# Performance work log

Measured on AMD Instinct MI355X. Metric: run time of the kernel, lower is better.

## Reference

```python
import jax, jax.numpy as jnp
import numpy as np
import math

B, S, D, H = 2, 2048, 1024, 16
HD = D // H            # head dim = 64
E, K = 8, 2            # routed experts, top-k
HM = 1024              # moe_inter_dim (multiple_of=256 keeps it)
HS = 1024              # shared expert hidden = moe_inter_dim * n_shared_experts
EPS = 1e-6
TEMP = 1.0


def setup_inputs() -> dict:
    key = jax.random.key(0)
    ks = jax.random.split(key, 16)
    s = 0.02
    x = jax.random.normal(ks[0], (B, S, D), jnp.float32)
    # RoPE angles: theta = 10000
    inv_freq = 1.0 / (10000.0 ** (np.arange(0, HD, 2, dtype=np.float32) / HD))  # (HD//2,)
    ang = np.arange(S, dtype=np.float32)[:, None] * inv_freq[None, :]           # (S, HD//2)
    freqs_cos = jnp.asarray(np.cos(ang))
    freqs_sin = jnp.asarray(np.sin(ang))
    return {
        "x": x,
        "freqs_cos": freqs_cos,
        "freqs_sin": freqs_sin,
        "att_norm_w": jnp.ones((D,), jnp.float32),
        "ffn_norm_w": jnp.ones((D,), jnp.float32),
        "wq": jax.random.normal(ks[1], (D, D), jnp.float32) * s,
        "wk": jax.random.normal(ks[2], (D, D), jnp.float32) * s,
        "wv": jax.random.normal(ks[3], (D, D), jnp.float32) * s,
        "wo": jax.random.normal(ks[4], (D, D), jnp.float32) * s,
        "gate_w": jax.random.normal(ks[5], (E, D), jnp.float32) * s,
        "ew1": jax.random.normal(ks[6], (E, D, HM), jnp.float32) * s,
        "ew2": jax.random.normal(ks[7], (E, HM, D), jnp.float32) * s,
        "ew3": jax.random.normal(ks[8], (E, D, HM), jnp.float32) * s,
        "sw1": jax.random.normal(ks[9], (D, HS), jnp.float32) * s,
        "sw2": jax.random.normal(ks[10], (HS, D), jnp.float32) * s,
        "sw3": jax.random.normal(ks[11], (D, HS), jnp.float32) * s,
    }


def _rmsnorm(x, w):
    return x * jax.lax.rsqrt(jnp.mean(x * x, axis=-1, keepdims=True) + EPS) * w


def _rope(t, cos, sin):
    # t: (B,H,S,HD); rotate pairs (even, odd) like complex multiply
    tr = t.reshape(B, H, S, HD // 2, 2)
    t0, t1 = tr[..., 0], tr[..., 1]
    c = cos[None, None, :, :]
    s_ = sin[None, None, :, :]
    o0 = t0 * c - t1 * s_
    o1 = t0 * s_ + t1 * c
    return jnp.stack([o0, o1], axis=-1).reshape(B, H, S, HD)


def reference(x, freqs_cos, freqs_sin, att_norm_w, ffn_norm_w,
              wq, wk, wv, wo, gate_w, ew1, ew2, ew3, sw1, sw2, sw3):
    # ---- attention sub-block ----
    xn = _rmsnorm(x, att_norm_w)
    q = (xn @ wq).reshape(B, S, H, HD).transpose(0, 2, 1, 3)  # (B,H,S,HD)
    k = (xn @ wk).reshape(B, S, H, HD).transpose(0, 2, 1, 3)
    v = (xn @ wv).reshape(B, S, H, HD).transpose(0, 2, 1, 3)
    q = _rope(q, freqs_cos, freqs_sin)
    k = _rope(k, freqs_cos, freqs_sin)
    scores = jnp.einsum('bhqd,bhkd->bhqk', q, k) / math.sqrt(HD)
    attn = jax.nn.softmax(scores, axis=-1)
    out = jnp.einsum('bhqk,bhkd->bhqd', attn, v)
    out = out.transpose(0, 2, 1, 3).reshape(B, S, D) @ wo
    h = x + out

    # ---- MoE sub-block ----
    xf = _rmsnorm(h, ffn_norm_w).reshape(-1, D)  # (N,D), N=B*S
    # shared expert (SwiGLU)
    shared = (jax.nn.silu(xf @ sw1) * (xf @ sw3)) @ sw2
    # gate (eval mode: no noise)
    g_scores = (xf @ gate_w.T) / TEMP
    probs = jax.nn.softmax(g_scores, axis=-1)          # (N,E)
    vals, idx = jax.lax.top_k(probs, K)                 # (N,K)
    vals = vals / (jnp.sum(vals, axis=-1, keepdims=True) + 1e-9)
    # per-token per-expert weight (equivalent to scatter into expert_mask)
    mask = jnp.sum(jax.nn.one_hot(idx, E, dtype=xf.dtype) * vals[..., None], axis=1)  # (N,E)
    # routed experts: dense per-expert SwiGLU, weighted combine (zero weight => no contribution)
    h1 = jax.nn.silu(jnp.einsum('nd,edh->enh', xf, ew1)) * jnp.einsum('nd,edh->enh', xf, ew3)
    eo = jnp.einsum('enh,ehd->end', h1, ew2)            # (E,N,D)
    y = jnp.einsum('end,ne->nd', eo, mask) + shared
    return h + y.reshape(B, S, D)
```

## Files before the change

kernel.cpp:

```cpp
#include <hip/hip_runtime.h>
#include <hip/hip_bf16.h>
#include <stdint.h>


typedef __hip_bfloat16 bf16;
typedef __attribute__((ext_vector_type(8))) __bf16 bf16x8;
typedef __attribute__((ext_vector_type(4))) float f32x4;
typedef __attribute__((ext_vector_type(2))) unsigned int u32x2;

#define S_  2048
#define D_  1024
#define N_  4096
#define HM_ 1024
#define HS_ 1024

__device__ __forceinline__ float b2f(bf16 h) { return __bfloat162float(h); }
__device__ __forceinline__ bf16  f2b(float f) { return __float2bfloat16(f); }

__device__ __forceinline__ bf16x8 ld_bf16x8(const bf16* p) {
    union { uint4 u; bf16x8 v; } x;
    x.u = *(const uint4*)p;
    return x.v;
}

__device__ __forceinline__ void gload_lds16(const void* gsrc, void* ldst) {
    __builtin_amdgcn_global_load_lds(
        (__attribute__((address_space(1))) void*)const_cast<void*>(gsrc),
        (__attribute__((address_space(3))) void*)ldst, 16, 0, 0);
}

__device__ __forceinline__ u32x2 tr16_read(unsigned lds_off) {
    u32x2 d;
    asm volatile("ds_read_b64_tr_b16 %0, %1" : "=v"(d) : "v"(lds_off));
    return d;
}

__global__ __launch_bounds__(256)
void transpose_cvt(const float* __restrict__ in, bf16* __restrict__ out,
                   int ld_in, int ld_out, int rowmul, int rowoff,
                   long in_bstride, long out_bstride)
{
    __shared__ float t[32][33];
    const int e = blockIdx.z;
    in  += (size_t)e * in_bstride;
    out += (size_t)e * out_bstride;
    const int c0 = blockIdx.x * 32, r0 = blockIdx.y * 32;
    const int tx = threadIdx.x & 31, ty = threadIdx.x >> 5;
#pragma unroll
    for (int i = 0; i < 32; i += 8)
        t[ty + i][tx] = in[(size_t)(r0 + ty + i) * ld_in + c0 + tx];
    __syncthreads();
#pragma unroll
    for (int i = 0; i < 32; i += 8)
        out[(size_t)((c0 + ty + i) * rowmul + rowoff) * ld_out + r0 + tx] = f2b(t[tx][ty + i]);
}

__global__ __launch_bounds__(256)
void rmsnorm_kernel(const float* __restrict__ x, const float* __restrict__ w,
                    bf16* __restrict__ out)
{
    const int n = blockIdx.x;
    const int tid = threadIdx.x;
    const float4 v = *(const float4*)(x + (size_t)n * D_ + tid * 4);
    float ss = v.x * v.x + v.y * v.y + v.z * v.z + v.w * v.w;
#pragma unroll
    for (int m = 1; m < 64; m <<= 1) ss += __shfl_xor(ss, m);
    __shared__ float red[4];
    if ((tid & 63) == 0) red[tid >> 6] = ss;
    __syncthreads();
    const float tot = red[0] + red[1] + red[2] + red[3];
    const float rstd = rsqrtf(tot * (1.0f / D_) + 1e-6f);
    const float4 wv = *(const float4*)(w + tid * 4);
    union { bf16 h[4]; uint2 u; } pk;
    pk.h[0] = f2b(v.x * rstd * wv.x);
    pk.h[1] = f2b(v.y * rstd * wv.y);
    pk.h[2] = f2b(v.z * rstd * wv.z);
    pk.h[3] = f2b(v.w * rstd * wv.w);
    *(uint2*)(out + (size_t)n * D_ + tid * 4) = pk.u;
}

template<int EPI, int MODE>
__global__ __launch_bounds__(256)
void gemm_bt(const bf16* __restrict__ A, const bf16* __restrict__ Bt,
             void* __restrict__ Cout, const float* __restrict__ resid,
             int M, int Kdim, int lda, int ldb, int ldc, long bstride,
             const int* __restrict__ tlist, const int* __restrict__ offs)
{
    __shared__ bf16 As[128 * 32];
    __shared__ bf16 Bs[128 * 32];
    const int tid = threadIdx.x;
    const int wave = tid >> 6, lane = tid & 63;

    int mcount = M, outBase = 0;
    const bf16* Bp = Bt;
    if (MODE != 0) {
        const int e = blockIdx.z;
        outBase = offs[e];
        mcount = offs[e + 1] - outBase;
        Bp = Bt + (size_t)e * bstride;
    }
    const int m0 = blockIdx.y * 128;
    if (m0 >= mcount) return;
    const int n0 = blockIdx.x * 128;

    const int srow = tid >> 2;
    const int scol = (tid & 3) * 8;
    const bf16* aptr[2];
    const bf16* bptr[2];
#pragma unroll
    for (int i = 0; i < 2; i++) {
        int r = m0 + i * 64 + srow;
        if (r >= mcount) r = mcount - 1;
        long arow;
        if (MODE == 1)      arow = tlist[outBase + r];
        else if (MODE == 2) arow = (long)outBase + r;
        else                arow = r;
        aptr[i] = A + (size_t)arow * lda + scol;
        bptr[i] = Bp + (size_t)(n0 + i * 64 + srow) * ldb + scol;
    }

    f32x4 zero4 = {0.f, 0.f, 0.f, 0.f};
    f32x4 acc[4][4];
#pragma unroll
    for (int m = 0; m < 4; m++)
#pragma unroll
        for (int n = 0; n < 4; n++) acc[m][n] = zero4;

    const int wm = (wave >> 1) * 64, wn = (wave & 1) * 64;
    const int fr = lane & 15, fk = (lane >> 4) * 8;
    const int aoff = (wm + fr) * 32 + fk;
    const int boff = (wn + fr) * 32 + fk;

    for (int kt = 0; kt < Kdim; kt += 32) {
        __syncthreads();
#pragma unroll
        for (int i = 0; i < 2; i++) {
            gload_lds16(aptr[i] + kt, (char*)As + i * 4096 + wave * 1024);
            gload_lds16(bptr[i] + kt, (char*)Bs + i * 4096 + wave * 1024);
        }
        __syncthreads();
        bf16x8 af[4], bfr[4];
#pragma unroll
        for (int m = 0; m < 4; m++) af[m] = ld_bf16x8(&As[aoff + m * 512]);
#pragma unroll
        for (int n = 0; n < 4; n++) bfr[n] = ld_bf16x8(&Bs[boff + n * 512]);
#pragma unroll
        for (int m = 0; m < 4; m++)
#pragma unroll
            for (int n = 0; n < 4; n++)
                acc[m][n] = __builtin_amdgcn_mfma_f32_16x16x32_bf16(af[m], bfr[n], acc[m][n], 0, 0, 0);
    }

    const int crow = m0 + wm + (lane >> 4) * 4;
    const int ccol = n0 + wn + fr;
#pragma unroll
    for (int m = 0; m < 4; m++)
#pragma unroll
        for (int n = 0; n < 4; n++)
#pragma unroll
            for (int j = 0; j < 4; j++) {
                const int r = crow + m * 16 + j;
                const int c = ccol + n * 16;
                const float v = acc[m][n][j];
                if (EPI == 3) {
                    const float other = __shfl_xor(v, 1);
                    const float res = (v / (1.f + __expf(-v))) * other;
                    if (((lane & 1) == 0) && r < mcount)
                        ((bf16*)Cout)[(size_t)(outBase + r) * ldc + (c >> 1)] = f2b(res);
                } else if (r < mcount) {
                    const size_t oi = (size_t)(outBase + r) * ldc + c;
                    if (EPI == 0)      ((bf16*)Cout)[oi] = f2b(v);
                    else if (EPI == 1) ((float*)Cout)[oi] = v;
                    else               ((float*)Cout)[oi] = resid[oi] + v;
                }
            }
}

__global__ __launch_bounds__(256)
void rope_kernel(bf16* __restrict__ qkv, const float* __restrict__ fc, const float* __restrict__ fs)
{
    const int n = blockIdx.x;
    const int s = n & (S_ - 1);
    bf16* row = qkv + (size_t)n * 3072;
    for (int p = threadIdx.x; p < 1024; p += 256) {
        const int sec = p >> 9;
        const int idx = p & 511;
        const int hh = idx >> 5, j = idx & 31;
        const int col = sec * 1024 + hh * 64 + 2 * j;
        const float c = fc[s * 32 + j], si = fs[s * 32 + j];
        const float v0 = b2f(row[col]), v1 = b2f(row[col + 1]);
        float o0 = v0 * c - v1 * si;
        float o1 = v0 * si + v1 * c;
        if (sec == 0) { o0 *= 0.125f; o1 *= 0.125f; }
        row[col] = f2b(o0);
        row[col + 1] = f2b(o1);
    }
}

__global__ __launch_bounds__(256)
void attn_kernel(const bf16* __restrict__ qkv, bf16* __restrict__ out)
{
    __shared__ __align__(16) bf16 Ks[64 * 72];
    __shared__ __align__(16) bf16 Vs[4 * 1032 + 8];
    const int tid = threadIdx.x, wave = tid >> 6, lane = tid & 63;
    const int b = blockIdx.z, hh = blockIdx.y;
    const int q0 = blockIdx.x * 128;
    const bf16* base  = qkv + ((size_t)b * S_) * 3072 + (size_t)hh * 64;
    const bf16* kbase = base + 1024;
    const bf16* vbase = base + 2048;
    const int fr = lane & 15, fg = lane >> 4;

    bf16x8 aq[2][2];
#pragma unroll
    for (int qb = 0; qb < 2; qb++)
#pragma unroll
        for (int s2 = 0; s2 < 2; s2++)
            aq[qb][s2] = ld_bf16x8(base + (size_t)(q0 + wave * 32 + qb * 16 + fr) * 3072 + s2 * 32 + fg * 8);

    f32x4 zero4 = {0.f, 0.f, 0.f, 0.f};
    f32x4 acc_o[2][4];
    float mrow[2], lrow[2];
#pragma unroll
    for (int qb = 0; qb < 2; qb++) {
#pragma unroll
        for (int hf = 0; hf < 4; hf++) acc_o[qb][hf] = zero4;
        mrow[qb] = -1e30f; lrow[qb] = 0.f;
    }

    const int srow = tid >> 2, sc4 = tid & 3;
    const unsigned vtr0 =
        (unsigned)(uintptr_t)(__attribute__((address_space(3))) void*)&Vs[0] + lane * 8;

    uint4 kg0, kg1, vg0, vg1;
    {
        const bf16* kr = kbase + (size_t)srow * 3072 + sc4 * 16;
        kg0 = *(const uint4*)kr; kg1 = *(const uint4*)(kr + 8);
        const bf16* vr = vbase + (size_t)srow * 3072 + sc4 * 16;
        vg0 = *(const uint4*)vr; vg1 = *(const uint4*)(vr + 8);
    }

    for (int kv0 = 0; kv0 < S_; kv0 += 64) {
        __syncthreads();
        *(uint4*)&Ks[srow * 72 + sc4 * 16]         = kg0;
        *(uint4*)&Ks[srow * 72 + sc4 * 16 + 8]     = kg1;
        *(uint4*)&Vs[sc4 * 1032 + srow * 16]       = vg0;
        *(uint4*)&Vs[sc4 * 1032 + srow * 16 + 8]   = vg1;
        __syncthreads();
        if (kv0 + 64 < S_) {
            const bf16* kr = kbase + (size_t)(kv0 + 64 + srow) * 3072 + sc4 * 16;
            kg0 = *(const uint4*)kr; kg1 = *(const uint4*)(kr + 8);
            const bf16* vr = vbase + (size_t)(kv0 + 64 + srow) * 3072 + sc4 * 16;
            vg0 = *(const uint4*)vr; vg1 = *(const uint4*)(vr + 8);
        }

        f32x4 sc[4][2];
#pragma unroll
        for (int kt = 0; kt < 4; kt++)
#pragma unroll
            for (int qb = 0; qb < 2; qb++) sc[kt][qb] = zero4;
        __builtin_amdgcn_s_setprio(1);
#pragma unroll
        for (int kt = 0; kt < 4; kt++) {
            const bf16x8 k0 = ld_bf16x8(&Ks[(kt * 16 + fr) * 72 + fg * 8]);
            const bf16x8 k1 = ld_bf16x8(&Ks[(kt * 16 + fr) * 72 + 32 + fg * 8]);
#pragma unroll
            for (int qb = 0; qb < 2; qb++) {
                sc[kt][qb] = __builtin_amdgcn_mfma_f32_16x16x32_bf16(k0, aq[qb][0], sc[kt][qb], 0, 0, 0);
                sc[kt][qb] = __builtin_amdgcn_mfma_f32_16x16x32_bf16(k1, aq[qb][1], sc[kt][qb], 0, 0, 0);
            }
        }
        __builtin_amdgcn_s_setprio(0);

        bf16x8 pcomb[2][2];
        float scalv[2];
#pragma unroll
        for (int qb = 0; qb < 2; qb++) {
            float pm = -1e30f;
#pragma unroll
            for (int kt = 0; kt < 4; kt++)
#pragma unroll
                for (int j = 0; j < 4; j++) pm = fmaxf(pm, sc[kt][qb][j]);
            pm = fmaxf(pm, __shfl_xor(pm, 16));
            pm = fmaxf(pm, __shfl_xor(pm, 32));
            const float mnew = fmaxf(mrow[qb], pm);
            const float scal = __expf(mrow[qb] - mnew);
            mrow[qb] = mnew;
            float ps = 0.f;
            union { bf16 h[16]; bf16x8 v8[2]; } pk;
#pragma unroll
            for (int kt = 0; kt < 4; kt++)
#pragma unroll
                for (int j = 0; j < 4; j++) {
                    const float p = __expf(sc[kt][qb][j] - mnew);
                    ps += p;
                    pk.h[kt * 4 + j] = f2b(p);
                }
            pcomb[qb][0] = pk.v8[0];
            pcomb[qb][1] = pk.v8[1];
            ps += __shfl_xor(ps, 16);
            ps += __shfl_xor(ps, 32);
            lrow[qb] = lrow[qb] * scal + ps;
            scalv[qb] = scal;
        }

#pragma unroll
        for (int j = 0; j < 4; j++) {
            const int src = (lane & 48) + fg * 4 + j;
            const float s0 = __shfl(scalv[0], src);
            const float s1 = __shfl(scalv[1], src);
#pragma unroll
            for (int hf = 0; hf < 4; hf++) {
                acc_o[0][hf][j] *= s0;
                acc_o[1][hf][j] *= s1;
            }
        }

#pragma unroll
        for (int tp = 0; tp < 2; tp++) {
            union { u32x2 d2[2]; bf16x8 v8; } vc[4];
#pragma unroll
            for (int hf = 0; hf < 4; hf++) {
                vc[hf].d2[0] = tr16_read(vtr0 + hf * 2064 + (tp * 2)     * 512);
                vc[hf].d2[1] = tr16_read(vtr0 + hf * 2064 + (tp * 2 + 1) * 512);
            }
            asm volatile("s_waitcnt lgkmcnt(0)" ::: "memory");
            __builtin_amdgcn_sched_barrier(0);
            __builtin_amdgcn_s_setprio(1);
#pragma unroll
            for (int hf = 0; hf < 4; hf++)
#pragma unroll
                for (int qb = 0; qb < 2; qb++)
                    acc_o[qb][hf] = __builtin_amdgcn_mfma_f32_16x16x32_bf16(
                        pcomb[qb][tp], vc[hf].v8, acc_o[qb][hf], 0, 0, 0);
            __builtin_amdgcn_s_setprio(0);
        }
    }

#pragma unroll
    for (int qb = 0; qb < 2; qb++) {
        const float inv = 1.f / lrow[qb];
#pragma unroll
        for (int j = 0; j < 4; j++) {
            const float ij = __shfl(inv, (lane & 48) + fg * 4 + j);
            const int r = q0 + wave * 32 + qb * 16 + fg * 4 + j;
#pragma unroll
            for (int hf = 0; hf < 4; hf++)
                out[((size_t)(b * S_ + r)) * D_ + hh * 64 + hf * 16 + fr] =
                    f2b(acc_o[qb][hf][j] * ij);
        }
    }
}

__global__ __launch_bounds__(256)
void gating_kernel(const float* __restrict__ h, const float* __restrict__ gw,
                   const float* __restrict__ wnorm,
                   int* __restrict__ top_idx, float* __restrict__ top_w)
{
    const int wave = threadIdx.x >> 6, lane = threadIdx.x & 63;
    const int n = blockIdx.x * 4 + wave;
    const float* hr = h + (size_t)n * D_;
    float acc[8] = {0.f, 0.f, 0.f, 0.f, 0.f, 0.f, 0.f, 0.f};
    float ss = 0.f;
    for (int d = lane * 4; d < D_; d += 256) {
        const float4 hv = *(const float4*)(hr + d);
        const float4 wv = *(const float4*)(wnorm + d);
        ss += hv.x * hv.x + hv.y * hv.y + hv.z * hv.z + hv.w * hv.w;
        const float x0 = hv.x * wv.x, x1 = hv.y * wv.y, x2 = hv.z * wv.z, x3 = hv.w * wv.w;
#pragma unroll
        for (int e2 = 0; e2 < 8; e2++) {
            const float4 gv = *(const float4*)(gw + e2 * D_ + d);
            acc[e2] += x0 * gv.x + x1 * gv.y + x2 * gv.z + x3 * gv.w;
        }
    }
#pragma unroll
    for (int m = 1; m < 64; m <<= 1) {
        ss += __shfl_xor(ss, m);
#pragma unroll
        for (int e2 = 0; e2 < 8; e2++) acc[e2] += __shfl_xor(acc[e2], m);
    }
    if (lane == 0) {
        const float rstd = rsqrtf(ss * (1.0f / D_) + 1e-6f);
        float s[8];
#pragma unroll
        for (int e2 = 0; e2 < 8; e2++) s[e2] = acc[e2] * rstd;
        int e0 = 0;
#pragma unroll
        for (int e2 = 1; e2 < 8; e2++) if (s[e2] > s[e0]) e0 = e2;
        int e1 = (e0 == 0) ? 1 : 0;
#pragma unroll
        for (int e2 = 0; e2 < 8; e2++) if (e2 != e0 && s[e2] > s[e1]) e1 = e2;
        const float mx = s[e0];
        float Z = 0.f;
        float p[8];
#pragma unroll
        for (int e2 = 0; e2 < 8; e2++) { p[e2] = __expf(s[e2] - mx); Z += p[e2]; }
        const float v0 = p[e0] / Z, v1 = p[e1] / Z;
        const float sm = v0 + v1 + 1e-9f;
        top_idx[n * 2] = e0; top_idx[n * 2 + 1] = e1;
        top_w[n * 2] = v0 / sm; top_w[n * 2 + 1] = v1 / sm;
    }
}

__global__ __launch_bounds__(1024)
void route_kernel(const int* __restrict__ top_idx, int* __restrict__ offs,
                  int* __restrict__ token_list, int* __restrict__ tok_pos)
{
    __shared__ int hist[8];
    __shared__ int base[8];
    const int tid = threadIdx.x;
    if (tid < 8) hist[tid] = 0;
    __syncthreads();
    int4 e4a = *(const int4*)(top_idx + tid * 8);
    int4 e4b = *(const int4*)(top_idx + tid * 8 + 4);
    int myidx[8] = {e4a.x, e4a.y, e4a.z, e4a.w, e4b.x, e4b.y, e4b.z, e4b.w};
#pragma unroll
    for (int i = 0; i < 8; i++) atomicAdd(&hist[myidx[i]], 1);
    __syncthreads();
    if (tid == 0) {
        int o = 0;
#pragma unroll
        for (int e = 0; e < 8; e++) { base[e] = o; offs[e] = o; o += hist[e]; }
        offs[8] = o;
    }
    __syncthreads();
    if (tid < 8) hist[tid] = 0;
    __syncthreads();
#pragma unroll
    for (int i = 0; i < 8; i++) {
        const int entry = tid * 8 + i;
        const int e = myidx[i];
        const int pos = base[e] + atomicAdd(&hist[e], 1);
        token_list[pos] = entry >> 1;
        tok_pos[entry] = pos;
    }
}

__global__ __launch_bounds__(256)
void combine_kernel(const float* __restrict__ h, const float* __restrict__ y,
                    const bf16* __restrict__ eo, const int* __restrict__ tok_pos,
                    const float* __restrict__ top_w, float* __restrict__ out)
{
    const int idx = blockIdx.x * 256 + threadIdx.x;
    const int n = idx >> 8;
    const int c = (idx & 255) * 4;
    const float4 hv = *(const float4*)(h + (size_t)n * D_ + c);
    const float4 yv = *(const float4*)(y + (size_t)n * D_ + c);
    const int p0 = tok_pos[n * 2], p1 = tok_pos[n * 2 + 1];
    const float w0 = top_w[n * 2], w1 = top_w[n * 2 + 1];
    union { uint2 u; bf16 hh[4]; } a0, a1;
    a0.u = *(const uint2*)(eo + (size_t)p0 * D_ + c);
    a1.u = *(const uint2*)(eo + (size_t)p1 * D_ + c);
    float4 r;
    r.x = hv.x + yv.x + w0 * b2f(a0.hh[0]) + w1 * b2f(a1.hh[0]);
    r.y = hv.y + yv.y + w0 * b2f(a0.hh[1]) + w1 * b2f(a1.hh[1]);
    r.z = hv.z + yv.z + w0 * b2f(a0.hh[2]) + w1 * b2f(a1.hh[2]);
    r.w = hv.w + yv.w + w0 * b2f(a0.hh[3]) + w1 * b2f(a1.hh[3]);
    *(float4*)(out + (size_t)n * D_ + c) = r;
}

extern "C" void kernel_launch(void* const* d_in, const int* in_sizes, int n_in,
                              void* d_out, int out_size, void* d_ws, size_t ws_size,
                              hipStream_t stream)
{
    const float* x   = (const float*)d_in[0];
    const float* fc  = (const float*)d_in[1];
    const float* fs  = (const float*)d_in[2];
    const float* anw = (const float*)d_in[3];
    const float* fnw = (const float*)d_in[4];
    const float* wq  = (const float*)d_in[5];
    const float* wk  = (const float*)d_in[6];
    const float* wv  = (const float*)d_in[7];
    const float* wo  = (const float*)d_in[8];
    const float* gw  = (const float*)d_in[9];
    const float* ew1 = (const float*)d_in[10];
    const float* ew2 = (const float*)d_in[11];
    const float* ew3 = (const float*)d_in[12];
    const float* sw1 = (const float*)d_in[13];
    const float* sw2 = (const float*)d_in[14];
    const float* sw3 = (const float*)d_in[15];

    char* ws = (char*)d_ws;
    bf16*  wqkv_t = (bf16*)(ws + 0);
    bf16*  wo_t   = (bf16*)(ws + 6291456);
    bf16*  sw13_t = (bf16*)(ws + 8388608);
    bf16*  sw2_t  = (bf16*)(ws + 12582912);
    bf16*  ew13_t = (bf16*)(ws + 14680064);
    bf16*  ew2_t  = (bf16*)(ws + 48234496);
    bf16*  xn     = (bf16*)(ws + 65011712);
    bf16*  qkv    = (bf16*)(ws + 73400320);
    bf16*  attn   = (bf16*)(ws + 98566144);
    float* hbuf   = (float*)(ws + 106954752);
    float* ybuf   = (float*)(ws + 123731968);
    bf16*  eo     = (bf16*)(ws + 140509184);
    char*  misc   = ws + 157286400;
    int*   offs       = (int*)(misc + 64);
    int*   top_idx    = (int*)(misc + 128);
    float* top_w      = (float*)(misc + 128 + 32768);
    int*   token_list = (int*)(misc + 128 + 65536);
    int*   tok_pos    = (int*)(misc + 128 + 98304);

    const dim3 tb(256);
    transpose_cvt<<<dim3(32, 32, 1), tb, 0, stream>>>(wq,  wqkv_t,              1024, 1024, 1, 0, 0, 0);
    transpose_cvt<<<dim3(32, 32, 1), tb, 0, stream>>>(wk,  wqkv_t + 1024*1024,  1024, 1024, 1, 0, 0, 0);
    transpose_cvt<<<dim3(32, 32, 1), tb, 0, stream>>>(wv,  wqkv_t + 2048*1024,  1024, 1024, 1, 0, 0, 0);
    transpose_cvt<<<dim3(32, 32, 1), tb, 0, stream>>>(wo,  wo_t,                1024, 1024, 1, 0, 0, 0);
    transpose_cvt<<<dim3(32, 32, 1), tb, 0, stream>>>(sw1, sw13_t,              1024, 1024, 2, 0, 0, 0);
    transpose_cvt<<<dim3(32, 32, 1), tb, 0, stream>>>(sw3, sw13_t,              1024, 1024, 2, 1, 0, 0);
    transpose_cvt<<<dim3(32, 32, 1), tb, 0, stream>>>(sw2, sw2_t,               1024, 1024, 1, 0, 0, 0);
    transpose_cvt<<<dim3(32, 32, 8), tb, 0, stream>>>(ew1, ew13_t,              1024, 1024, 2, 0, 1048576, 2097152);
    transpose_cvt<<<dim3(32, 32, 8), tb, 0, stream>>>(ew3, ew13_t,              1024, 1024, 2, 1, 1048576, 2097152);
    transpose_cvt<<<dim3(32, 32, 8), tb, 0, stream>>>(ew2, ew2_t,               1024, 1024, 1, 0, 1048576, 1048576);

    rmsnorm_kernel<<<N_, tb, 0, stream>>>(x, anw, xn);
    gemm_bt<0, 0><<<dim3(24, 32, 1), tb, 0, stream>>>(xn, wqkv_t, qkv, nullptr,
        N_, 1024, 1024, 1024, 3072, 0, nullptr, nullptr);
    rope_kernel<<<N_, tb, 0, stream>>>(qkv, fc, fs);
    attn_kernel<<<dim3(16, 16, 2), tb, 0, stream>>>(qkv, attn);
    gemm_bt<2, 0><<<dim3(8, 32, 1), tb, 0, stream>>>(attn, wo_t, hbuf, x,
        N_, 1024, 1024, 1024, 1024, 0, nullptr, nullptr);

    rmsnorm_kernel<<<N_, tb, 0, stream>>>(hbuf, fnw, xn);
    gating_kernel<<<N_ / 4, tb, 0, stream>>>(hbuf, gw, fnw, top_idx, top_w);
    route_kernel<<<1, 1024, 0, stream>>>(top_idx, offs, token_list, tok_pos);

    gemm_bt<3, 0><<<dim3(16, 32, 1), tb, 0, stream>>>(xn, sw13_t, attn, nullptr,
        N_, 1024, 1024, 1024, 1024, 0, nullptr, nullptr);
    gemm_bt<1, 0><<<dim3(8, 32, 1), tb, 0, stream>>>(attn, sw2_t, ybuf, nullptr,
        N_, 1024, 1024, 1024, 1024, 0, nullptr, nullptr);

    gemm_bt<3, 1><<<dim3(16, 32, 8), tb, 0, stream>>>(xn, ew13_t, qkv, nullptr,
        0, 1024, 1024, 1024, 1024, 2097152, token_list, offs);
    gemm_bt<0, 2><<<dim3(8, 32, 8), tb, 0, stream>>>((const bf16*)qkv, ew2_t, eo, nullptr,
        0, 1024, 1024, 1024, 1024, 1048576, nullptr, offs);

    combine_kernel<<<4096, tb, 0, stream>>>(hbuf, ybuf, eo, tok_pos, top_w, (float*)d_out);
}
```

Before: 418.3 us.

## Double-buffer GEMM LDS, swizzle blocks, fold shared expert into grouped expert GEMM

The GEMM now double-buffers its A/B tiles in LDS, prefetching the next K slice before computing the current one, and uses a single barrier per iteration. Workgroup indices are swizzled to improve L2 locality. The shared expert is appended as a ninth expert in the grouped GEMMs, with an identity token list, which removes two separate launches and the fp32 intermediate buffer. The shared expert output is now stored in bf16, which reduces precision, and LDS use per block doubles, which may lower occupancy.

```diff
diff --git a/kernel.cpp b/kernel.cpp
--- a/kernel.cpp
+++ b/kernel.cpp
@@ -11,8 +11,6 @@
 #define S_  2048
 #define D_  1024
 #define N_  4096
-#define HM_ 1024
-#define HS_ 1024
 
 __device__ __forceinline__ float b2f(bf16 h) { return __bfloat162float(h); }
 __device__ __forceinline__ bf16  f2b(float f) { return __float2bfloat16(f); }
@@ -86,10 +84,19 @@
              int M, int Kdim, int lda, int ldb, int ldc, long bstride,
              const int* __restrict__ tlist, const int* __restrict__ offs)
 {
-    __shared__ bf16 As[128 * 32];
-    __shared__ bf16 Bs[128 * 32];
+    __shared__ bf16 As[2][128 * 32];
+    __shared__ bf16 Bs[2][128 * 32];
     const int tid = threadIdx.x;
     const int wave = tid >> 6, lane = tid & 63;
+
+    int bx, by;
+    {
+        const int gx = gridDim.x;
+        const int nwg = gx * gridDim.y;
+        int flat = blockIdx.y * gx + blockIdx.x;
+        flat = (flat & 7) * (nwg >> 3) + (flat >> 3);
+        bx = flat % gx; by = flat / gx;
+    }
 
     int mcount = M, outBase = 0;
     const bf16* Bp = Bt;
@@ -99,9 +106,9 @@
         mcount = offs[e + 1] - outBase;
         Bp = Bt + (size_t)e * bstride;
     }
-    const int m0 = blockIdx.y * 128;
+    const int m0 = by * 128;
     if (m0 >= mcount) return;
-    const int n0 = blockIdx.x * 128;
+    const int n0 = bx * 128;
 
     const int srow = tid >> 2;
     const int scol = (tid & 3) * 8;
@@ -131,24 +138,38 @@
     const int aoff = (wm + fr) * 32 + fk;
     const int boff = (wn + fr) * 32 + fk;
 
-    for (int kt = 0; kt < Kdim; kt += 32) {
-        __syncthreads();
-#pragma unroll
-        for (int i = 0; i < 2; i++) {
-            gload_lds16(aptr[i] + kt, (char*)As + i * 4096 + wave * 1024);
-            gload_lds16(bptr[i] + kt, (char*)Bs + i * 4096 + wave * 1024);
-        }
-        __syncthreads();
+    const int nkt = Kdim >> 5;
+#pragma unroll
+    for (int i = 0; i < 2; i++) {
+        gload_lds16(aptr[i], (char*)&As[0][0] + i * 4096 + wave * 1024);
+        gload_lds16(bptr[i], (char*)&Bs[0][0] + i * 4096 + wave * 1024);
+    }
+    __syncthreads();
+
+    int p = 0;
+    for (int kt = 0; kt < nkt; kt++) {
+        if (kt + 1 < nkt) {
+            const int ko = (kt + 1) * 32;
+#pragma unroll
+            for (int i = 0; i < 2; i++) {
+                gload_lds16(aptr[i] + ko, (char*)&As[p ^ 1][0] + i * 4096 + wave * 1024);
+                gload_lds16(bptr[i] + ko, (char*)&Bs[p ^ 1][0] + i * 4096 + wave * 1024);
+            }
+        }
+        const bf16* Ab = &As[p][0];
+        const bf16* Bb = &Bs[p][0];
         bf16x8 af[4], bfr[4];
 #pragma unroll
-        for (int m = 0; m < 4; m++) af[m] = ld_bf16x8(&As[aoff + m * 512]);
-#pragma unroll
-        for (int n = 0; n < 4; n++) bfr[n] = ld_bf16x8(&Bs[boff + n * 512]);
+        for (int m = 0; m < 4; m++) af[m] = ld_bf16x8(&Ab[aoff + m * 512]);
+#pragma unroll
+        for (int n = 0; n < 4; n++) bfr[n] = ld_bf16x8(&Bb[boff + n * 512]);
 #pragma unroll
         for (int m = 0; m < 4; m++)
 #pragma unroll
             for (int n = 0; n < 4; n++)
                 acc[m][n] = __builtin_amdgcn_mfma_f32_16x16x32_bf16(af[m], bfr[n], acc[m][n], 0, 0, 0);
+        __syncthreads();
+        p ^= 1;
     }
 
     const int crow = m0 + wm + (lane >> 4) * 4;
@@ -421,6 +442,7 @@
 #pragma unroll
         for (int e = 0; e < 8; e++) { base[e] = o; offs[e] = o; o += hist[e]; }
         offs[8] = o;
+        offs[9] = o + N_;
     }
     __syncthreads();
     if (tid < 8) hist[tid] = 0;
@@ -433,28 +455,31 @@
         token_list[pos] = entry >> 1;
         tok_pos[entry] = pos;
     }
-}
-
-__global__ __launch_bounds__(256)
-void combine_kernel(const float* __restrict__ h, const float* __restrict__ y,
-                    const bf16* __restrict__ eo, const int* __restrict__ tok_pos,
-                    const float* __restrict__ top_w, float* __restrict__ out)
+#pragma unroll
+    for (int i = 0; i < 4; i++)
+        token_list[2 * N_ + tid * 4 + i] = tid * 4 + i;
+}
+
+__global__ __launch_bounds__(256)
+void combine_kernel(const float* __restrict__ h, const bf16* __restrict__ eo,
+                    const int* __restrict__ tok_pos, const float* __restrict__ top_w,
+                    float* __restrict__ out)
 {
     const int idx = blockIdx.x * 256 + threadIdx.x;
     const int n = idx >> 8;
     const int c = (idx & 255) * 4;
     const float4 hv = *(const float4*)(h + (size_t)n * D_ + c);
-    const float4 yv = *(const float4*)(y + (size_t)n * D_ + c);
     const int p0 = tok_pos[n * 2], p1 = tok_pos[n * 2 + 1];
     const float w0 = top_w[n * 2], w1 = top_w[n * 2 + 1];
-    union { uint2 u; bf16 hh[4]; } a0, a1;
-    a0.u = *(const uint2*)(eo + (size_t)p0 * D_ + c);
-    a1.u = *(const uint2*)(eo + (size_t)p1 * D_ + c);
+    union { uint2 u; bf16 hh[4]; } a0, a1, ash;
+    a0.u  = *(const uint2*)(eo + (size_t)p0 * D_ + c);
+    a1.u  = *(const uint2*)(eo + (size_t)p1 * D_ + c);
+    ash.u = *(const uint2*)(eo + (size_t)(2 * N_ + n) * D_ + c);
     float4 r;
-    r.x = hv.x + yv.x + w0 * b2f(a0.hh[0]) + w1 * b2f(a1.hh[0]);
-    r.y = hv.y + yv.y + w0 * b2f(a0.hh[1]) + w1 * b2f(a1.hh[1]);
-    r.z = hv.z + yv.z + w0 * b2f(a0.hh[2]) + w1 * b2f(a1.hh[2]);
-    r.w = hv.w + yv.w + w0 * b2f(a0.hh[3]) + w1 * b2f(a1.hh[3]);
+    r.x = hv.x + b2f(ash.hh[0]) + w0 * b2f(a0.hh[0]) + w1 * b2f(a1.hh[0]);
+    r.y = hv.y + b2f(ash.hh[1]) + w0 * b2f(a0.hh[1]) + w1 * b2f(a1.hh[1]);
+    r.z = hv.z + b2f(ash.hh[2]) + w0 * b2f(a0.hh[2]) + w1 * b2f(a1.hh[2]);
+    r.w = hv.w + b2f(ash.hh[3]) + w0 * b2f(a0.hh[3]) + w1 * b2f(a1.hh[3]);
     *(float4*)(out + (size_t)n * D_ + c) = r;
 }
 
@@ -482,34 +507,31 @@
     char* ws = (char*)d_ws;
     bf16*  wqkv_t = (bf16*)(ws + 0);
     bf16*  wo_t   = (bf16*)(ws + 6291456);
-    bf16*  sw13_t = (bf16*)(ws + 8388608);
-    bf16*  sw2_t  = (bf16*)(ws + 12582912);
-    bf16*  ew13_t = (bf16*)(ws + 14680064);
-    bf16*  ew2_t  = (bf16*)(ws + 48234496);
+    bf16*  ew13_t = (bf16*)(ws + 8388608);
+    bf16*  ew2_t  = (bf16*)(ws + 46137344);
     bf16*  xn     = (bf16*)(ws + 65011712);
     bf16*  qkv    = (bf16*)(ws + 73400320);
     bf16*  attn   = (bf16*)(ws + 98566144);
     float* hbuf   = (float*)(ws + 106954752);
-    float* ybuf   = (float*)(ws + 123731968);
-    bf16*  eo     = (bf16*)(ws + 140509184);
-    char*  misc   = ws + 157286400;
-    int*   offs       = (int*)(misc + 64);
+    bf16*  eo     = (bf16*)(ws + 123731968);
+    char*  misc   = ws + 148897792;
+    int*   offs       = (int*)(misc + 0);
     int*   top_idx    = (int*)(misc + 128);
     float* top_w      = (float*)(misc + 128 + 32768);
     int*   token_list = (int*)(misc + 128 + 65536);
-    int*   tok_pos    = (int*)(misc + 128 + 98304);
+    int*   tok_pos    = (int*)(misc + 128 + 131072);
 
     const dim3 tb(256);
     transpose_cvt<<<dim3(32, 32, 1), tb, 0, stream>>>(wq,  wqkv_t,              1024, 1024, 1, 0, 0, 0);
     transpose_cvt<<<dim3(32, 32, 1), tb, 0, stream>>>(wk,  wqkv_t + 1024*1024,  1024, 1024, 1, 0, 0, 0);
     transpose_cvt<<<dim3(32, 32, 1), tb, 0, stream>>>(wv,  wqkv_t + 2048*1024,  1024, 1024, 1, 0, 0, 0);
     transpose_cvt<<<dim3(32, 32, 1), tb, 0, stream>>>(wo,  wo_t,                1024, 1024, 1, 0, 0, 0);
-    transpose_cvt<<<dim3(32, 32, 1), tb, 0, stream>>>(sw1, sw13_t,              1024, 1024, 2, 0, 0, 0);
-    transpose_cvt<<<dim3(32, 32, 1), tb, 0, stream>>>(sw3, sw13_t,              1024, 1024, 2, 1, 0, 0);
-    transpose_cvt<<<dim3(32, 32, 1), tb, 0, stream>>>(sw2, sw2_t,               1024, 1024, 1, 0, 0, 0);
     transpose_cvt<<<dim3(32, 32, 8), tb, 0, stream>>>(ew1, ew13_t,              1024, 1024, 2, 0, 1048576, 2097152);
     transpose_cvt<<<dim3(32, 32, 8), tb, 0, stream>>>(ew3, ew13_t,              1024, 1024, 2, 1, 1048576, 2097152);
     transpose_cvt<<<dim3(32, 32, 8), tb, 0, stream>>>(ew2, ew2_t,               1024, 1024, 1, 0, 1048576, 1048576);
+    transpose_cvt<<<dim3(32, 32, 1), tb, 0, stream>>>(sw1, ew13_t + 8*2097152,  1024, 1024, 2, 0, 0, 0);
+    transpose_cvt<<<dim3(32, 32, 1), tb, 0, stream>>>(sw3, ew13_t + 8*2097152,  1024, 1024, 2, 1, 0, 0);
+    transpose_cvt<<<dim3(32, 32, 1), tb, 0, stream>>>(sw2, ew2_t  + 8*1048576,  1024, 1024, 1, 0, 0, 0);
 
     rmsnorm_kernel<<<N_, tb, 0, stream>>>(x, anw, xn);
     gemm_bt<0, 0><<<dim3(24, 32, 1), tb, 0, stream>>>(xn, wqkv_t, qkv, nullptr,
@@ -523,15 +545,10 @@
     gating_kernel<<<N_ / 4, tb, 0, stream>>>(hbuf, gw, fnw, top_idx, top_w);
     route_kernel<<<1, 1024, 0, stream>>>(top_idx, offs, token_list, tok_pos);
 
-    gemm_bt<3, 0><<<dim3(16, 32, 1), tb, 0, stream>>>(xn, sw13_t, attn, nullptr,
-        N_, 1024, 1024, 1024, 1024, 0, nullptr, nullptr);
-    gemm_bt<1, 0><<<dim3(8, 32, 1), tb, 0, stream>>>(attn, sw2_t, ybuf, nullptr,
-        N_, 1024, 1024, 1024, 1024, 0, nullptr, nullptr);
-
-    gemm_bt<3, 1><<<dim3(16, 32, 8), tb, 0, stream>>>(xn, ew13_t, qkv, nullptr,
+    gemm_bt<3, 1><<<dim3(16, 32, 9), tb, 0, stream>>>(xn, ew13_t, qkv, nullptr,
         0, 1024, 1024, 1024, 1024, 2097152, token_list, offs);
-    gemm_bt<0, 2><<<dim3(8, 32, 8), tb, 0, stream>>>((const bf16*)qkv, ew2_t, eo, nullptr,
+    gemm_bt<0, 2><<<dim3(8, 32, 9), tb, 0, stream>>>((const bf16*)qkv, ew2_t, eo, nullptr,
         0, 1024, 1024, 1024, 1024, 1048576, nullptr, offs);
 
-    combine_kernel<<<4096, tb, 0, stream>>>(hbuf, ybuf, eo, tok_pos, top_w, (float*)d_out);
-}
+    combine_kernel<<<4096, tb, 0, stream>>>(hbuf, eo, tok_pos, top_w, (float*)d_out);
+}
```

New measurement: 551.8 us. 1.32x slower.
